# Kernel optimization log

Hardware: AMD Instinct MI355X
Metric: run time of the kernel (lower is better)

Reference implementation:

```python
import jax, jax.numpy as jnp
import numpy as np

L, H, P = 8192, 1024, 512
DT_MIN, DT_MAX = 1e-3, 1e-1
CONJ_SYM = True


def setup_inputs() -> dict:
    key = jax.random.key(0)
    ks = jax.random.split(key, 6)
    input_sequence = jax.random.normal(ks[0], (L, H), jnp.float32)
    # HiPPO-DPLR-like eigenvalues: negative real part, linearly spaced imag part
    Lambda_re = -0.5 * jnp.ones((P,), jnp.float32)
    Lambda_im = jnp.pi * jnp.arange(P, dtype=jnp.float32)
    # B param stacks real/imag in last dim: (P, H, 2); C: (H, P, 2)
    B = jax.random.normal(ks[1], (P, H, 2), jnp.float32) / np.float32(np.sqrt(2 * H))
    C = jax.random.normal(ks[2], (H, P, 2), jnp.float32) / np.float32(np.sqrt(2 * P))
    D = jax.random.normal(ks[3], (H,), jnp.float32)
    log_step = jax.random.uniform(ks[4], (P,), jnp.float32,
                                  minval=np.float32(np.log(DT_MIN)),
                                  maxval=np.float32(np.log(DT_MAX)))
    return dict(input_sequence=input_sequence, Lambda_re=Lambda_re,
                Lambda_im=Lambda_im, B=B, C=C, D=D, log_step=log_step)


def _binop(e_i, e_j):
    # diagonal LTI composition: (A, b) o (A', b') = (A'A, A'b + b')
    A_i, b_i = e_i
    A_j, b_j = e_j
    return A_j * A_i, A_j * b_i + b_j


def _forward(input_sequence, Lambda_re, Lambda_im, B, C, D, log_step):
    Lambda = Lambda_re + 1j * Lambda_im                  # (P,) complex
    B_tilde = B[..., 0] + 1j * B[..., 1]                 # (P, H)
    C_tilde = C[..., 0] + 1j * C[..., 1]                 # (H, P)
    step = jnp.exp(log_step)                             # (P,)  step_rescale = 1.0
    # ZOH discretization
    Lambda_bar = jnp.exp(Lambda * step)                  # (P,)
    B_bar = ((1.0 / Lambda) * (Lambda_bar - 1.0))[:, None] * B_tilde  # (P, H)
    # input projection, vectorized over L: Bu[l] = B_bar @ u[l]
    Bu = input_sequence.astype(B_bar.dtype) @ B_bar.T    # (L, P) complex
    Lambda_elems = jnp.broadcast_to(Lambda_bar, Bu.shape)  # (L, P)
    _, xs = jax.lax.associative_scan(_binop, (Lambda_elems, Bu))  # states (L, P)
    mult = 2.0 if CONJ_SYM else 1.0
    ys = mult * jnp.einsum('lp,hp->lh', xs, C_tilde).real  # (L, H)
    out = ys + D * input_sequence                          # D-skip
    return out, xs[-1]


def reference(input_sequence, Lambda_re, Lambda_im, B, C, D, log_step):
    return _forward(input_sequence, Lambda_re, Lambda_im, B, C, D, log_step)
```

## Files before the change

kernel.cpp:

```cpp
#include <hip/hip_runtime.h>
#include <hip/hip_bf16.h>
#include <hip/hip_fp16.h>
#include <stdint.h>

typedef _Float16 f16;
typedef __attribute__((ext_vector_type(8))) _Float16 half8;
typedef __attribute__((ext_vector_type(4))) _Float16 half4;
typedef __attribute__((ext_vector_type(4))) float f32x4;

#define L_SEQ 8192
#define H_DIM 1024
#define P_DIM 512
#define NB 256
#define TT 32

#define GL16(gp, lp)                                                        \
  __builtin_amdgcn_global_load_lds(                                          \
      (const __attribute__((address_space(1))) void*)(gp),                   \
      (__attribute__((address_space(3))) void*)(lp), 16, 0, 0)

__global__ void k_consts(const float* __restrict__ lre, const float* __restrict__ lim,
                         const float* __restrict__ lstep, float* __restrict__ cst) {
  int p = threadIdx.x;
  double step = exp((double)lstep[p]);
  double ar = (double)lre[p] * step, ai = (double)lim[p] * step;
  double er = exp(ar);
  double lbr = er * cos(ai), lbi = er * sin(ai);
  double nr = lbr - 1.0, ni = lbi;
  double d = (double)lre[p] * (double)lre[p] + (double)lim[p] * (double)lim[p];
  double gr = (nr * (double)lre[p] + ni * (double)lim[p]) / d;
  double gi = (ni * (double)lre[p] - nr * (double)lim[p]) / d;
  cst[p] = (float)lbr; cst[512 + p] = (float)lbi;
  cst[1024 + p] = (float)gr; cst[1536 + p] = (float)gi;
#pragma unroll
  for (int s = 0; s < 8; ++s) {
    double n = 32.0 * (double)(1 << s);
    double eT = exp(ar * n);
    cst[3072 + s * 1024 + p]       = (float)(eT * cos(ai * n));
    cst[3072 + s * 1024 + 512 + p] = (float)(eT * sin(ai * n));
  }
  double gm = fmax(fabs(gr), fabs(gi));
  int e = ilogb(gm) + 1;
  float sc = ldexpf(1.0f, e);
  cst[11264 + p] = sc;
  cst[11264 + 512 + p] = sc;
  cst[12288 + p] = ldexpf(1.0f, -e);
}

__global__ void k_prep(const float* __restrict__ B, const float* __restrict__ C,
                       const float* __restrict__ u, const float* __restrict__ cst,
                       f16* __restrict__ W1, f16* __restrict__ W2,
                       f16* __restrict__ uh) {
  int blk = blockIdx.x;
  if (blk < 4096) {
    int idx = blk * 256 + threadIdx.x;
    int n = idx >> 10, k = idx & 1023;
    int p = n & 511;
    float b0 = B[(size_t)(p * 1024 + k) * 2];
    float b1 = B[(size_t)(p * 1024 + k) * 2 + 1];
    float gr = cst[1024 + p], gi = cst[1536 + p];
    float inv = cst[12288 + p];
    float re = (gr * b0 - gi * b1) * inv;
    float im = (gr * b1 + gi * b0) * inv;
    W1[idx] = (f16)((n < 512) ? re : im);
  } else if (blk < 8192) {
    int idx = (blk - 4096) * 256 + threadIdx.x;
    int h = idx >> 10, k = idx & 1023;
    float v = (k < 512) ? 2.0f * C[(size_t)(h * 512 + k) * 2]
                        : -2.0f * C[(size_t)(h * 512 + (k - 512)) * 2 + 1];
    W2[idx] = (f16)v;
  } else {
    int i = (blk - 8192) * 256 + threadIdx.x;
    float4 v = reinterpret_cast<const float4*>(u)[i];
    half4 h;
    h.x = (f16)v.x; h.y = (f16)v.y; h.z = (f16)v.z; h.w = (f16)v.w;
    reinterpret_cast<half4*>(uh)[i] = h;
  }
}

template <int EPI>
__global__ __launch_bounds__(256) void k_gemm(const f16* __restrict__ A,
                                              const f16* __restrict__ Bm,
                                              float* __restrict__ CmF,
                                              f16* __restrict__ CmH,
                                              const float* __restrict__ D,
                                              const f16* __restrict__ Uh,
                                              const float* __restrict__ S) {
  __shared__ f16 As[128 * 32];
  __shared__ f16 Bs[128 * 32];
  const int tid = threadIdx.x;
  const int wave = tid >> 6, lane = tid & 63;
  const int bm = blockIdx.x >> 3, bn = blockIdx.x & 7;
  const int m0 = bm * 128, n0 = bn * 128;
  const int wr = (wave >> 1) * 64, wc = (wave & 1) * 64;
  const int lr = lane & 15, lg = lane >> 4;
  f32x4 acc[4][4] = {};

  const int c0 = wave * 64 + lane;
  const int c1 = c0 + 256;
  const int ar0 = c0 >> 2, ak0 = (c0 & 3) * 8;
  const int ar1 = c1 >> 2, ak1 = (c1 & 3) * 8;
  char* lA0 = (char*)As + wave * 1024;
  char* lA1 = (char*)As + 4096 + wave * 1024;
  char* lB0 = (char*)Bs + wave * 1024;
  char* lB1 = (char*)Bs + 4096 + wave * 1024;

  for (int kt = 0; kt < 32; ++kt) {
    const int k0 = kt * 32;
    GL16(A + (size_t)(m0 + ar0) * 1024 + k0 + ak0, lA0);
    GL16(A + (size_t)(m0 + ar1) * 1024 + k0 + ak1, lA1);
    GL16(Bm + (size_t)(n0 + ar0) * 1024 + k0 + ak0, lB0);
    GL16(Bm + (size_t)(n0 + ar1) * 1024 + k0 + ak1, lB1);
    __syncthreads();
    half8 af[4], bf[4];
#pragma unroll
    for (int m = 0; m < 4; ++m)
      af[m] = *(const half8*)&As[(wr + m * 16 + lr) * 32 + lg * 8];
#pragma unroll
    for (int n = 0; n < 4; ++n)
      bf[n] = *(const half8*)&Bs[(wc + n * 16 + lr) * 32 + lg * 8];
#pragma unroll
    for (int m = 0; m < 4; ++m)
#pragma unroll
      for (int n = 0; n < 4; ++n)
        acc[m][n] = __builtin_amdgcn_mfma_f32_16x16x32_f16(af[m], bf[n], acc[m][n], 0, 0, 0);
    __syncthreads();
  }

#pragma unroll
  for (int m = 0; m < 4; ++m)
#pragma unroll
    for (int n = 0; n < 4; ++n) {
      int row = m0 + wr + m * 16 + lg * 4;
      int col = n0 + wc + n * 16 + lr;
      float scale = (EPI == 0) ? S[col] : 0.0f;
#pragma unroll
      for (int j = 0; j < 4; ++j) {
        float v = acc[m][n][j];
        if (EPI) {
          v += D[col] * (float)Uh[(size_t)(row + j) * 1024 + col];
          CmF[(size_t)(row + j) * 1024 + col] = v;
        } else {
          CmH[(size_t)(row + j) * 1024 + col] = (f16)(v * scale);
        }
      }
    }
}

__global__ void k_scanA(const f16* __restrict__ Bu, const float* __restrict__ cst,
                        float* __restrict__ carry) {
  int p = threadIdx.x;
  int b = blockIdx.x;
  float lbr = cst[p], lbi = cst[512 + p];
  float xr = 0.f, xi = 0.f;
  const f16* row = Bu + (size_t)b * TT * 1024;
  for (int t = 0; t < TT; ++t) {
    float br = (float)row[t * 1024 + p], bi = (float)row[t * 1024 + 512 + p];
    float nxr = lbr * xr - lbi * xi + br;
    float nxi = lbr * xi + lbi * xr + bi;
    xr = nxr; xi = nxi;
  }
  carry[b * 1024 + p] = xr;
  carry[b * 1024 + 512 + p] = xi;
}

__global__ void k_scanB(const float* __restrict__ carry, const float* __restrict__ cst,
                        float* __restrict__ prefix) {
  __shared__ float sre[256], sim[256];
  int p = blockIdx.x;
  int b = threadIdx.x;
  float xr = carry[b * 1024 + p], xi = carry[b * 1024 + 512 + p];
  sre[b] = xr; sim[b] = xi;
  __syncthreads();
#pragma unroll
  for (int s = 0; s < 8; ++s) {
    float pr = cst[3072 + s * 1024 + p];
    float pi = cst[3072 + s * 1024 + 512 + p];
    int off = 1 << s;
    float ar = 0.f, ai = 0.f;
    if (b >= off) { ar = sre[b - off]; ai = sim[b - off]; }
    __syncthreads();
    xr += pr * ar - pi * ai;
    xi += pr * ai + pi * ar;
    sre[b] = xr; sim[b] = xi;
    __syncthreads();
  }
  float er = 0.f, ei = 0.f;
  if (b > 0) { er = sre[b - 1]; ei = sim[b - 1]; }
  prefix[b * 1024 + p] = er;
  prefix[b * 1024 + 512 + p] = ei;
}

__global__ void k_scanC(const f16* __restrict__ Bu, const float* __restrict__ cst,
                        const float* __restrict__ prefix, f16* __restrict__ X,
                        float* __restrict__ fin, int tail) {
  int p = threadIdx.x;
  int b = blockIdx.x;
  float lbr = cst[p], lbi = cst[512 + p];
  float xr = prefix[b * 1024 + p], xi = prefix[b * 1024 + 512 + p];
  const f16* row = Bu + (size_t)b * TT * 1024;
  f16* xrow = X + (size_t)b * TT * 1024;
  for (int t = 0; t < TT; ++t) {
    float br = (float)row[t * 1024 + p], bi = (float)row[t * 1024 + 512 + p];
    float nxr = lbr * xr - lbi * xi + br;
    float nxi = lbr * xi + lbi * xr + bi;
    xr = nxr; xi = nxi;
    xrow[t * 1024 + p] = (f16)xr;
    xrow[t * 1024 + 512 + p] = (f16)xi;
  }
  if (b == NB - 1) {
    if (tail >= 1024) {
      fin[2 * p] = xr;
      fin[2 * p + 1] = xi;
    } else if (tail >= 512) {
      fin[p] = xr;
    }
  }
}

extern "C" void kernel_launch(void* const* d_in, const int* in_sizes, int n_in,
                              void* d_out, int out_size, void* d_ws, size_t ws_size,
                              hipStream_t stream) {
  const float* u    = (const float*)d_in[0];
  const float* lre  = (const float*)d_in[1];
  const float* lim  = (const float*)d_in[2];
  const float* B    = (const float*)d_in[3];
  const float* C    = (const float*)d_in[4];
  const float* D    = (const float*)d_in[5];
  const float* lstp = (const float*)d_in[6];
  float* out = (float*)d_out;
  int tail = out_size - L_SEQ * H_DIM;

  char* ws = (char*)d_ws;
  float* cst   = (float*)(ws + 0);
  f16* uh      = (f16*)(ws + 65536);
  f16* W1      = (f16*)(ws + 16842752);
  f16* W2      = (f16*)(ws + 18939904);
  f16* Bu      = (f16*)(ws + 21037056);
  f16* Xc      = (f16*)(ws + 37814272);
  float* carry = (float*)(ws + 54591488);
  float* prefix= (float*)(ws + 55639040);

  k_consts<<<1, 512, 0, stream>>>(lre, lim, lstp, cst);
  k_prep<<<16384, 256, 0, stream>>>(B, C, u, cst, W1, W2, uh);
  k_gemm<0><<<512, 256, 0, stream>>>(uh, W1, nullptr, Bu, nullptr, nullptr, cst + 11264);
  k_scanA<<<NB, 512, 0, stream>>>(Bu, cst, carry);
  k_scanB<<<512, 256, 0, stream>>>(carry, cst, prefix);
  k_scanC<<<NB, 512, 0, stream>>>(Bu, cst, prefix, Xc, out + (size_t)L_SEQ * H_DIM, tail);
  k_gemm<1><<<512, 256, 0, stream>>>(Xc, W2, out, nullptr, D, uh, nullptr);
}
```

Before: 184.1 us.

## Widen GEMM K-tile with XOR-swizzled LDS and fold carry scan into scanC

The GEMM K-tile doubles from 32 to 64, so there are half as many barrier pairs per output tile. The LDS layout uses an XOR swizzle on 16-byte chunks to avoid bank conflicts on the wider rows. Separately, the k_scanB block-level Hillis-Steele prefix kernel is removed. Each k_scanC block now serially folds all earlier chunk carries using the lambda^32 power, which saves one launch and the prefix buffer. The cost is O(b) redundant serial work per block, up to 255 steps for the last blocks, which adds load imbalance and repeated carry reads.

```diff
diff --git a/kernel.cpp b/kernel.cpp
--- a/kernel.cpp
+++ b/kernel.cpp
@@ -32,12 +32,10 @@
   double gi = (ni * (double)lre[p] - nr * (double)lim[p]) / d;
   cst[p] = (float)lbr; cst[512 + p] = (float)lbi;
   cst[1024 + p] = (float)gr; cst[1536 + p] = (float)gi;
-#pragma unroll
-  for (int s = 0; s < 8; ++s) {
-    double n = 32.0 * (double)(1 << s);
-    double eT = exp(ar * n);
-    cst[3072 + s * 1024 + p]       = (float)(eT * cos(ai * n));
-    cst[3072 + s * 1024 + 512 + p] = (float)(eT * sin(ai * n));
+  {
+    double eT = exp(ar * 32.0);
+    cst[3072 + p] = (float)(eT * cos(ai * 32.0));
+    cst[3584 + p] = (float)(eT * sin(ai * 32.0));
   }
   double gm = fmax(fabs(gr), fabs(gi));
   int e = ilogb(gm) + 1;
@@ -86,8 +84,8 @@
                                               const float* __restrict__ D,
                                               const f16* __restrict__ Uh,
                                               const float* __restrict__ S) {
-  __shared__ f16 As[128 * 32];
-  __shared__ f16 Bs[128 * 32];
+  __shared__ f16 As[128 * 64];
+  __shared__ f16 Bs[128 * 64];
   const int tid = threadIdx.x;
   const int wave = tid >> 6, lane = tid & 63;
   const int bm = blockIdx.x >> 3, bn = blockIdx.x & 7;
@@ -96,34 +94,46 @@
   const int lr = lane & 15, lg = lane >> 4;
   f32x4 acc[4][4] = {};
 
-  const int c0 = wave * 64 + lane;
-  const int c1 = c0 + 256;
-  const int ar0 = c0 >> 2, ak0 = (c0 & 3) * 8;
-  const int ar1 = c1 >> 2, ak1 = (c1 & 3) * 8;
-  char* lA0 = (char*)As + wave * 1024;
-  char* lA1 = (char*)As + 4096 + wave * 1024;
-  char* lB0 = (char*)Bs + wave * 1024;
-  char* lB1 = (char*)Bs + 4096 + wave * 1024;
-
-  for (int kt = 0; kt < 32; ++kt) {
-    const int k0 = kt * 32;
-    GL16(A + (size_t)(m0 + ar0) * 1024 + k0 + ak0, lA0);
-    GL16(A + (size_t)(m0 + ar1) * 1024 + k0 + ak1, lA1);
-    GL16(Bm + (size_t)(n0 + ar0) * 1024 + k0 + ak0, lB0);
-    GL16(Bm + (size_t)(n0 + ar1) * 1024 + k0 + ak1, lB1);
+  int srow[4], scol[4];
+#pragma unroll
+  for (int w = 0; w < 4; ++w) {
+    int c = w * 256 + tid;
+    srow[w] = c >> 3;
+    scol[w] = ((c & 7) * 8) ^ ((srow[w] & 7) << 3);
+  }
+
+  for (int kt = 0; kt < 16; ++kt) {
+    const int k0 = kt * 64;
+#pragma unroll
+    for (int w = 0; w < 4; ++w) {
+      GL16(A + (size_t)(m0 + srow[w]) * 1024 + k0 + scol[w],
+           (char*)As + (w * 256 + wave * 64) * 16);
+      GL16(Bm + (size_t)(n0 + srow[w]) * 1024 + k0 + scol[w],
+           (char*)Bs + (w * 256 + wave * 64) * 16);
+    }
     __syncthreads();
-    half8 af[4], bf[4];
-#pragma unroll
-    for (int m = 0; m < 4; ++m)
-      af[m] = *(const half8*)&As[(wr + m * 16 + lr) * 32 + lg * 8];
-#pragma unroll
-    for (int n = 0; n < 4; ++n)
-      bf[n] = *(const half8*)&Bs[(wc + n * 16 + lr) * 32 + lg * 8];
-#pragma unroll
-    for (int m = 0; m < 4; ++m)
-#pragma unroll
-      for (int n = 0; n < 4; ++n)
-        acc[m][n] = __builtin_amdgcn_mfma_f32_16x16x32_f16(af[m], bf[n], acc[m][n], 0, 0, 0);
+    half8 af[2][4], bf[2][4];
+#pragma unroll
+    for (int m = 0; m < 4; ++m) {
+      int ra = wr + m * 16 + lr;
+      int sw = (ra & 7) << 4;
+      af[0][m] = *(const half8*)((const char*)As + ra * 128 + ((lg * 16) ^ sw));
+      af[1][m] = *(const half8*)((const char*)As + ra * 128 + ((64 + lg * 16) ^ sw));
+    }
+#pragma unroll
+    for (int n = 0; n < 4; ++n) {
+      int rb = wc + n * 16 + lr;
+      int sw = (rb & 7) << 4;
+      bf[0][n] = *(const half8*)((const char*)Bs + rb * 128 + ((lg * 16) ^ sw));
+      bf[1][n] = *(const half8*)((const char*)Bs + rb * 128 + ((64 + lg * 16) ^ sw));
+    }
+#pragma unroll
+    for (int h = 0; h < 2; ++h)
+#pragma unroll
+      for (int m = 0; m < 4; ++m)
+#pragma unroll
+        for (int n = 0; n < 4; ++n)
+          acc[m][n] = __builtin_amdgcn_mfma_f32_16x16x32_f16(af[h][m], bf[h][n], acc[m][n], 0, 0, 0);
     __syncthreads();
   }
 
@@ -164,40 +174,20 @@
   carry[b * 1024 + 512 + p] = xi;
 }
 
-__global__ void k_scanB(const float* __restrict__ carry, const float* __restrict__ cst,
-                        float* __restrict__ prefix) {
-  __shared__ float sre[256], sim[256];
-  int p = blockIdx.x;
-  int b = threadIdx.x;
-  float xr = carry[b * 1024 + p], xi = carry[b * 1024 + 512 + p];
-  sre[b] = xr; sim[b] = xi;
-  __syncthreads();
-#pragma unroll
-  for (int s = 0; s < 8; ++s) {
-    float pr = cst[3072 + s * 1024 + p];
-    float pi = cst[3072 + s * 1024 + 512 + p];
-    int off = 1 << s;
-    float ar = 0.f, ai = 0.f;
-    if (b >= off) { ar = sre[b - off]; ai = sim[b - off]; }
-    __syncthreads();
-    xr += pr * ar - pi * ai;
-    xi += pr * ai + pi * ar;
-    sre[b] = xr; sim[b] = xi;
-    __syncthreads();
-  }
-  float er = 0.f, ei = 0.f;
-  if (b > 0) { er = sre[b - 1]; ei = sim[b - 1]; }
-  prefix[b * 1024 + p] = er;
-  prefix[b * 1024 + 512 + p] = ei;
-}
-
 __global__ void k_scanC(const f16* __restrict__ Bu, const float* __restrict__ cst,
-                        const float* __restrict__ prefix, f16* __restrict__ X,
+                        const float* __restrict__ carry, f16* __restrict__ X,
                         float* __restrict__ fin, int tail) {
   int p = threadIdx.x;
   int b = blockIdx.x;
+  float l32r = cst[3072 + p], l32i = cst[3584 + p];
+  float xr = 0.f, xi = 0.f;
+  for (int j = 0; j < b; ++j) {
+    float cr = carry[j * 1024 + p], ci = carry[j * 1024 + 512 + p];
+    float nr = l32r * xr - l32i * xi + cr;
+    float ni = l32r * xi + l32i * xr + ci;
+    xr = nr; xi = ni;
+  }
   float lbr = cst[p], lbi = cst[512 + p];
-  float xr = prefix[b * 1024 + p], xi = prefix[b * 1024 + 512 + p];
   const f16* row = Bu + (size_t)b * TT * 1024;
   f16* xrow = X + (size_t)b * TT * 1024;
   for (int t = 0; t < TT; ++t) {
@@ -239,13 +229,11 @@
   f16* Bu      = (f16*)(ws + 21037056);
   f16* Xc      = (f16*)(ws + 37814272);
   float* carry = (float*)(ws + 54591488);
-  float* prefix= (float*)(ws + 55639040);
 
   k_consts<<<1, 512, 0, stream>>>(lre, lim, lstp, cst);
   k_prep<<<16384, 256, 0, stream>>>(B, C, u, cst, W1, W2, uh);
   k_gemm<0><<<512, 256, 0, stream>>>(uh, W1, nullptr, Bu, nullptr, nullptr, cst + 11264);
   k_scanA<<<NB, 512, 0, stream>>>(Bu, cst, carry);
-  k_scanB<<<512, 256, 0, stream>>>(carry, cst, prefix);
-  k_scanC<<<NB, 512, 0, stream>>>(Bu, cst, prefix, Xc, out + (size_t)L_SEQ * H_DIM, tail);
+  k_scanC<<<NB, 512, 0, stream>>>(Bu, cst, carry, Xc, out + (size_t)L_SEQ * H_DIM, tail);
   k_gemm<1><<<512, 256, 0, stream>>>(Xc, W2, out, nullptr, D, uh, nullptr);
 }
```

After: 227.6 us. 23.6% more time.
